# Kernel optimization log

Hardware: AMD Instinct MI355X
Metric: run time of the kernel (lower is better)

## Reference

```python
import jax, jax.numpy as jnp
import numpy as np

DN = ('NCHW', 'OIHW', 'NCHW')

def conv2d(x, w, b):
    y = jax.lax.conv_general_dilated(x, w, window_strides=(1, 1), padding='VALID', dimension_numbers=DN)
    return y + b[None, :, None, None]

def setup_inputs() -> dict:
    key = jax.random.key(0)
    ks = jax.random.split(key, 16)
    s = 0.02  # small init scale to keep relu chains numerically tame
    B, Cin, OUT = 128, 4, 9
    return {
        'state_m': jax.random.normal(ks[0], (B, Cin, 100, 100), jnp.float32),
        'state_g': jax.random.normal(ks[1], (B, 2), jnp.float32),
        'state_v': jax.random.normal(ks[2], (B, 2), jnp.float32),
        'conv1_w': jax.random.normal(ks[3], (32, Cin, 32, 32), jnp.float32) * s,
        'conv1_b': jnp.zeros((32,), jnp.float32),
        'conv2_w': jax.random.normal(ks[4], (64, 32, 32, 32), jnp.float32) * s,
        'conv2_b': jnp.zeros((64,), jnp.float32),
        'conv3_w': jax.random.normal(ks[5], (64, 64, 8, 8), jnp.float32) * s,
        'conv3_b': jnp.zeros((64,), jnp.float32),
        'conv4_w': jax.random.normal(ks[6], (64, 64, 8, 8), jnp.float32) * s,
        'conv4_b': jnp.zeros((64,), jnp.float32),
        'fc1_w': jax.random.normal(ks[7], (67, 4), jnp.float32) * s,
        'fc1_b': jnp.zeros((67,), jnp.float32),
        'fc2_w': jax.random.normal(ks[8], (512, 6400), jnp.float32) * s,
        'fc2_b': jnp.zeros((512,), jnp.float32),
        'fc3_w': jax.random.normal(ks[9], (512, 512), jnp.float32) * s,
        'fc3_b': jnp.zeros((512,), jnp.float32),
        'fc4_ea_w': jax.random.normal(ks[10], (OUT, 512), jnp.float32) * s,
        'fc4_ea_b': jnp.zeros((OUT,), jnp.float32),
        'fc4_ev_w': jax.random.normal(ks[11], (1, 512), jnp.float32) * s,
        'fc4_ev_b': jnp.zeros((1,), jnp.float32),
    }

def reference(state_m, state_g, state_v,
              conv1_w, conv1_b, conv2_w, conv2_b, conv3_w, conv3_b, conv4_w, conv4_b,
              fc1_w, fc1_b, fc2_w, fc2_b, fc3_w, fc3_b,
              fc4_ea_w, fc4_ea_b, fc4_ev_w, fc4_ev_b):
    x_m = jax.nn.relu(conv2d(state_m, conv1_w, conv1_b))   # [B,32,69,69]
    x_m = jax.nn.relu(conv2d(x_m, conv2_w, conv2_b))       # [B,64,38,38]
    x_m = jax.nn.relu(conv2d(x_m, conv3_w, conv3_b))       # [B,64,31,31]
    x_gv_ = jax.nn.relu(jnp.concatenate([state_g, state_v], axis=1) @ fc1_w.T + fc1_b)  # [B,67]
    convw = x_m.shape[2]  # 31
    # Torch loop overwrites x_gv each iteration: final tile is filled with x_gv_[0, convw-1]
    scalar = x_gv_[0, convw - 1]
    x_pls = x_m + scalar  # broadcast add (the CPU round-trip tile in torch)
    x_pls = jax.nn.relu(conv2d(x_pls, conv4_w, conv4_b))   # [B,64,24,24]
    x_pls = jax.nn.relu(conv2d(x_pls, conv4_w, conv4_b))   # [B,64,17,17]
    x_pls = jax.nn.relu(conv2d(x_pls, conv4_w, conv4_b))   # [B,64,10,10]
    x = x_pls.reshape(x_pls.shape[0], -1)                  # [B,6400]
    x = jax.nn.relu(x @ fc2_w.T + fc2_b)
    x = jax.nn.relu(x @ fc3_w.T + fc3_b)
    adv = x @ fc4_ea_w.T + fc4_ea_b                        # [B,outputs]
    val = x @ fc4_ev_w.T + fc4_ev_b                        # [B,1]
    return adv + val - jnp.mean(adv, axis=1, keepdims=True)
```

## Files before the change

### kernel.cpp

```cpp
#include <hip/hip_runtime.h>
#include <stdint.h>


using bf16_t = __bf16;
using bf16x8 = __attribute__((ext_vector_type(8))) __bf16;
using bf16x4 = __attribute__((ext_vector_type(4))) __bf16;
using f32x4  = __attribute__((ext_vector_type(4))) float;
using f32x16 = __attribute__((ext_vector_type(16))) float;

__device__ __forceinline__ f32x4 mfma16(bf16x8 a, bf16x8 b, f32x4 c) {
    return __builtin_amdgcn_mfma_f32_16x16x32_bf16(a, b, c, 0, 0, 0);
}
__device__ __forceinline__ f32x16 mfma32(bf16x8 a, bf16x8 b, f32x16 c) {
    return __builtin_amdgcn_mfma_f32_32x32x16_bf16(a, b, c, 0, 0, 0);
}

template<bool A16>
__device__ __forceinline__ bf16x8 load_frag(const bf16_t* p) {
    if constexpr (A16) {
        return *reinterpret_cast<const bf16x8*>(p);
    } else {
        union { bf16x8 v; uint64_t u[2]; } r;
        r.u[0] = *reinterpret_cast<const uint64_t*>(p);
        r.u[1] = *reinterpret_cast<const uint64_t*>(p + 4);
        return r.v;
    }
}

template<int CIN>
__global__ void pack_w(const float* __restrict__ src, bf16_t* __restrict__ dst,
                       int COUT, int KK) {
    int total = COUT * KK;
    for (int t = blockIdx.x * blockDim.x + threadIdx.x; t < total;
         t += gridDim.x * blockDim.x) {
        int cout = t / KK;
        int khw  = t - cout * KK;
        alignas(16) bf16_t tmp[CIN];
        #pragma unroll
        for (int c = 0; c < CIN; ++c)
            tmp[c] = (bf16_t)src[((size_t)cout * CIN + c) * KK + khw];
        bf16_t* d = dst + (size_t)t * CIN;
        if constexpr (CIN == 1) {
            d[0] = tmp[0];
        } else if constexpr (CIN == 4) {
            *reinterpret_cast<uint2*>(d) = *reinterpret_cast<const uint2*>(tmp);
        } else {
            #pragma unroll
            for (int c = 0; c < CIN; c += 8)
                *reinterpret_cast<uint4*>(d + c) =
                    *reinterpret_cast<const uint4*>(tmp + c);
        }
    }
}

template<int CIN, int COUT, int K>
__global__ void pack_wA(const float* __restrict__ src, bf16_t* __restrict__ dst) {
    constexpr int S  = K * CIN / 16;
    constexpr int NT = COUT / 32;
    int t = blockIdx.x * 256 + threadIdx.x;
    int l  = t & 63;
    int f  = t >> 6;
    int n  = f % NT;
    int fs = f / NT;
    int s  = fs % S;
    int kh = fs / S;
    if (kh >= K) return;
    int cout = n * 32 + (l & 31);
    int k0   = s * 16 + (l >> 5) * 8;
    alignas(16) bf16_t tmp[8];
    #pragma unroll
    for (int e = 0; e < 8; ++e) {
        int k   = k0 + e;
        int kw  = k / CIN;
        int cin = k % CIN;
        tmp[e] = (bf16_t)src[(((size_t)cout * CIN + cin) * K + kh) * K + kw];
    }
    *reinterpret_cast<uint4*>(dst + (size_t)t * 8) =
        *reinterpret_cast<const uint4*>(tmp);
}

__global__ void fc1_scalar(const float* __restrict__ g, const float* __restrict__ v,
                           const float* __restrict__ w, const float* __restrict__ b,
                           float* __restrict__ outp) {
    if (threadIdx.x == 0 && blockIdx.x == 0) {
        float s = b[30] + g[0] * w[120] + g[1] * w[121] + v[0] * w[122] + v[1] * w[123];
        *outp = s > 0.f ? s : 0.f;
    }
}

template<int CIN, int COUT, int W, int K, int OW, int WMT, int NSLOT,
         int ADD_SCALAR>
__global__ __launch_bounds__(256, 2) void conv_rr(
    const bf16_t* __restrict__ in, const bf16_t* __restrict__ wA,
    const float* __restrict__ bias, bf16_t* __restrict__ out,
    const float* __restrict__ scal) {
    constexpr int  P     = OW * OW;
    constexpr int  PIXB  = CIN * 2;
    constexpr int  ROWB  = W * PIXB;
    constexpr bool TR    = (CIN >= 16);
    constexpr int  NCH   = TR ? PIXB / 16 : 1;
    constexpr int  SPP   = TR ? NCH / 2 : 1;
    constexpr int  PS    = TR ? (W + 1) * 16 : 0;
    constexpr int  SLOTB = TR ? NCH * PS : ROWB;
    constexpr int  LDSB  = NSLOT * SLOTB;
    constexpr int  S     = K * CIN / 16;
    constexpr int  NT    = COUT / 32;
    constexpr int  BPX   = WMT * 32 * 4;
    constexpr int  CH    = ROWB / 16;
    constexpr int  NLD   = (CH + 255) / 256;
    __shared__ __align__(16) char smem[LDSB];

    const int tid  = threadIdx.x;
    const int wave = tid >> 6, lane = tid & 63;
    const int l31  = lane & 31, h = lane >> 5;
    const int img  = blockIdx.z;
    const int p0   = blockIdx.x * BPX;

    const char* inb = (const char*)(in + (size_t)img * ((size_t)W * W * CIN));

    const int r0 = p0 / OW;
    int plast = p0 + BPX - 1; if (plast > P - 1) plast = P - 1;
    const int r1 = plast / OW;

    int woff[NLD];
    #pragma unroll
    for (int i = 0; i < NLD; ++i) {
        int c = i * 256 + tid;
        if (c < CH) woff[i] = TR ? (c % NCH) * PS + (c / NCH) * 16 : c * 16;
        else        woff[i] = 0;
    }

    int pix[WMT], ldsadr[WMT];
    #pragma unroll
    for (int m = 0; m < WMT; ++m) {
        int p  = p0 + (wave * WMT + m) * 32 + l31;
        pix[m] = p;
        int pc = p < P ? p : P - 1;
        int oh = pc / OW;
        int ow = pc - oh * OW;
        ldsadr[m] = (oh % NSLOT) * SLOTB +
                    (TR ? ow * 16 + h * PS : ow * PIXB + h * 16);
    }

    for (int r = r0; r <= r1; ++r) {
        const char* g = inb + (size_t)r * ROWB;
        int base = (r % NSLOT) * SLOTB;
        for (int c = tid; c < CH; c += 256) {
            bf16x8 v = *reinterpret_cast<const bf16x8*>(g + c * 16);
            int off = TR ? (c % NCH) * PS + (c / NCH) * 16 : c * 16;
            *reinterpret_cast<bf16x8*>(smem + base + off) = v;
        }
    }
    __syncthreads();

    f32x16 acc[WMT][NT] = {};

    int wsl = (r1 + 1) % NSLOT;
    const char* gpre = inb + (size_t)(r1 + 1) * ROWB;
    const bf16_t* wl = wA + lane * 8;

    for (int kh = 0; kh < K; ++kh) {
        bf16x8 stv[NLD];
        const bool pf = kh < K - 1;
        if (pf) {
            #pragma unroll
            for (int i = 0; i < NLD; ++i) {
                int c = i * 256 + tid;
                if (c < CH) stv[i] = *reinterpret_cast<const bf16x8*>(gpre + c * 16);
            }
        }
        const bf16_t* ap = wl + (size_t)kh * (S * NT * 512);

        auto bread = [&](int m, int s) -> bf16x8 {
            int a = TR ? ldsadr[m] + (s % SPP) * (2 * PS) + (s / SPP) * 16
                       : ldsadr[m] + s * 32;
            return *reinterpret_cast<const bf16x8*>(smem + a);
        };
        bf16x8 bcur[WMT], acur[NT];
        #pragma unroll
        for (int m = 0; m < WMT; ++m) bcur[m] = bread(m, 0);
        #pragma unroll
        for (int n = 0; n < NT; ++n)
            acur[n] = *reinterpret_cast<const bf16x8*>(ap + n * 512);

        #pragma unroll 8
        for (int s = 0; s < S - 1; ++s) {
            bf16x8 bnx[WMT], anx[NT];
            #pragma unroll
            for (int m = 0; m < WMT; ++m) bnx[m] = bread(m, s + 1);
            #pragma unroll
            for (int n = 0; n < NT; ++n)
                anx[n] = *reinterpret_cast<const bf16x8*>(ap + ((s + 1) * NT + n) * 512);
            #pragma unroll
            for (int m = 0; m < WMT; ++m)
                #pragma unroll
                for (int n = 0; n < NT; ++n)
                    acc[m][n] = mfma32(acur[n], bcur[m], acc[m][n]);
            #pragma unroll
            for (int m = 0; m < WMT; ++m) bcur[m] = bnx[m];
            #pragma unroll
            for (int n = 0; n < NT; ++n) acur[n] = anx[n];
        }
        #pragma unroll
        for (int m = 0; m < WMT; ++m)
            #pragma unroll
            for (int n = 0; n < NT; ++n)
                acc[m][n] = mfma32(acur[n], bcur[m], acc[m][n]);

        if (pf) {
            int wb0 = wsl * SLOTB;
            #pragma unroll
            for (int i = 0; i < NLD; ++i) {
                int c = i * 256 + tid;
                if (c < CH)
                    *reinterpret_cast<bf16x8*>(smem + wb0 + woff[i]) = stv[i];
            }
            gpre += ROWB;
            wsl = (wsl + 1 == NSLOT) ? 0 : wsl + 1;
        }
        __syncthreads();
        #pragma unroll
        for (int m = 0; m < WMT; ++m) {
            int a2 = ldsadr[m] + SLOTB;
            ldsadr[m] = a2 >= LDSB ? a2 - LDSB : a2;
        }
    }

    float sc = 0.f;
    if constexpr (ADD_SCALAR) sc = *scal;
    bf16_t* outb = out + (size_t)img * ((size_t)P * COUT);
    #pragma unroll
    for (int m = 0; m < WMT; ++m) {
        if (pix[m] < P) {
            #pragma unroll
            for (int n = 0; n < NT; ++n) {
                #pragma unroll
                for (int rg = 0; rg < 4; ++rg) {
                    int cb = n * 32 + rg * 8 + h * 4;
                    f32x4 bv = *reinterpret_cast<const f32x4*>(bias + cb);
                    union { bf16x4 v; uint2 u; } o;
                    #pragma unroll
                    for (int j = 0; j < 4; ++j) {
                        float x = acc[m][n][rg * 4 + j] + bv[j];
                        x = x > 0.f ? x : 0.f;
                        x += sc;
                        o.v[j] = (bf16_t)x;
                    }
                    *reinterpret_cast<uint2*>(outb + (size_t)pix[m] * COUT + cb) = o.u;
                }
            }
        }
    }
}

template<int CIN, int COUT, int W, int K, int OW, int NBLK, int WMT,
         int ADD_SCALAR, bool A16>
__global__ __launch_bounds__(256, 2) void conv_mfma(
    const bf16_t* __restrict__ in, const bf16_t* __restrict__ wp,
    const float* __restrict__ bias, bf16_t* __restrict__ out,
    const float* __restrict__ scal) {
    constexpr int P    = OW * OW;
    constexpr int KCIN = K * CIN;
    constexpr int KTOT = K * KCIN;
    constexpr int RS   = KCIN / 32;
    constexpr int NT   = NBLK / 16;
    constexpr int BMT  = WMT * 4;

    const int b     = blockIdx.z;
    const int cout0 = blockIdx.y * NBLK;
    const int wave  = threadIdx.x >> 6;
    const int lane  = threadIdx.x & 63;
    const int l15   = lane & 15;
    const int l4    = lane >> 4;
    const int mt0   = blockIdx.x * BMT + wave * WMT;

    const bf16_t* inb = in + (size_t)b * (W * W * CIN);

    int      pix[WMT];
    uint32_t pb[WMT];
    #pragma unroll
    for (int m = 0; m < WMT; ++m) {
        int p  = (mt0 + m) * 16 + l15;
        pix[m] = p;
        int pc = p < P ? p : P - 1;
        int oh = pc / OW;
        int ow = pc - oh * OW;
        pb[m]  = (uint32_t)(oh * W + ow) * CIN;
    }
    uint32_t wb[NT];
    #pragma unroll
    for (int n = 0; n < NT; ++n)
        wb[n] = (uint32_t)(cout0 + n * 16 + l15) * KTOT + (uint32_t)l4 * 8u;

    f32x4 acc[WMT][NT];
    #pragma unroll
    for (int m = 0; m < WMT; ++m)
        #pragma unroll
        for (int n = 0; n < NT; ++n)
            acc[m][n] = f32x4{0.f, 0.f, 0.f, 0.f};

    uint32_t bofs = (uint32_t)l4 * 8u;
    for (int kh = 0; kh < K; ++kh) {
        #pragma unroll
        for (int s = 0; s < RS; ++s) {
            bf16x8 af[NT];
            #pragma unroll
            for (int n = 0; n < NT; ++n)
                af[n] = load_frag<true>(wp + wb[n] + kh * KCIN + s * 32);
            #pragma unroll
            for (int m = 0; m < WMT; ++m) {
                bf16x8 bfr = load_frag<A16>(inb + pb[m] + bofs + s * 32);
                #pragma unroll
                for (int n = 0; n < NT; ++n)
                    acc[m][n] = mfma16(af[n], bfr, acc[m][n]);
            }
        }
        bofs += (uint32_t)(W * CIN);
    }

    float sc = 0.f;
    if constexpr (ADD_SCALAR) sc = *scal;
    bf16_t* outb = out + (size_t)b * P * COUT;
    #pragma unroll
    for (int n = 0; n < NT; ++n) {
        const int cb = cout0 + n * 16 + l4 * 4;
        f32x4 bv = *reinterpret_cast<const f32x4*>(bias + cb);
        #pragma unroll
        for (int m = 0; m < WMT; ++m) {
            if (pix[m] < P) {
                f32x4 v = acc[m][n];
                union { bf16x4 h; uint2 u; } st;
                #pragma unroll
                for (int r = 0; r < 4; ++r) {
                    float x = v[r] + bv[r];
                    x = x > 0.f ? x : 0.f;
                    x += sc;
                    st.h[r] = (bf16_t)x;
                }
                *reinterpret_cast<uint2*>(outb + (size_t)pix[m] * COUT + cb) = st.u;
            }
        }
    }
}

__global__ __launch_bounds__(256, 2) void fc2_kernel(
    const bf16_t* __restrict__ x, const bf16_t* __restrict__ w,
    float* __restrict__ part) {
    const int nb = blockIdx.x, kc = blockIdx.y;
    const int wave = threadIdx.x >> 6, lane = threadIdx.x & 63;
    const int l15 = lane & 15, l4 = lane >> 4;
    const int wm = wave & 1, wn = wave >> 1;

    f32x4 acc[4][2];
    #pragma unroll
    for (int m = 0; m < 4; ++m)
        #pragma unroll
        for (int n = 0; n < 2; ++n) acc[m][n] = f32x4{0.f, 0.f, 0.f, 0.f};

    uint32_t xb[4], wbf[2];
    #pragma unroll
    for (int m = 0; m < 4; ++m)
        xb[m] = (uint32_t)(16 * (wm * 4 + m) + l15) * 6400u + kc * 1600u + l4 * 8u;
    #pragma unroll
    for (int n = 0; n < 2; ++n)
        wbf[n] = (uint32_t)(nb * 64 + wn * 32 + n * 16 + l15) * 6400u + kc * 1600u + l4 * 8u;

    for (int s = 0; s < 50; ++s) {
        bf16x8 af[2];
        #pragma unroll
        for (int n = 0; n < 2; ++n)
            af[n] = load_frag<true>(w + wbf[n] + s * 32);
        #pragma unroll
        for (int m = 0; m < 4; ++m) {
            bf16x8 bfr = load_frag<true>(x + xb[m] + s * 32);
            #pragma unroll
            for (int n = 0; n < 2; ++n)
                acc[m][n] = mfma16(af[n], bfr, acc[m][n]);
        }
    }
    #pragma unroll
    for (int m = 0; m < 4; ++m) {
        int bcol = 16 * (wm * 4 + m) + l15;
        #pragma unroll
        for (int n = 0; n < 2; ++n) {
            int cf = nb * 64 + wn * 32 + n * 16 + l4 * 4;
            *reinterpret_cast<f32x4*>(part + ((size_t)kc * 128 + bcol) * 512 + cf) =
                acc[m][n];
        }
    }
}

__global__ void fc2_reduce(const float* __restrict__ part,
                           const float* __restrict__ bias,
                           bf16_t* __restrict__ xo) {
    int t = blockIdx.x * 256 + threadIdx.x;
    if (t < 128 * 512) {
        int b = t >> 9, co = t & 511;
        float s = bias[co];
        #pragma unroll
        for (int kc = 0; kc < 4; ++kc) s += part[((size_t)kc * 128 + b) * 512 + co];
        xo[t] = (bf16_t)(s > 0.f ? s : 0.f);
    }
}

__global__ __launch_bounds__(256, 2) void fc3_kernel(
    const bf16_t* __restrict__ x, const bf16_t* __restrict__ w,
    const float* __restrict__ bias, bf16_t* __restrict__ xo) {
    const int nb = blockIdx.x;
    const int wave = threadIdx.x >> 6, lane = threadIdx.x & 63;
    const int l15 = lane & 15, l4 = lane >> 4;

    f32x4 acc[2][4];
    #pragma unroll
    for (int m = 0; m < 2; ++m)
        #pragma unroll
        for (int n = 0; n < 4; ++n) acc[m][n] = f32x4{0.f, 0.f, 0.f, 0.f};

    uint32_t xb[2], wbf[4];
    #pragma unroll
    for (int m = 0; m < 2; ++m)
        xb[m] = (uint32_t)(16 * (wave * 2 + m) + l15) * 512u + l4 * 8u;
    #pragma unroll
    for (int n = 0; n < 4; ++n)
        wbf[n] = (uint32_t)(nb * 64 + n * 16 + l15) * 512u + l4 * 8u;

    #pragma unroll
    for (int s = 0; s < 16; ++s) {
        bf16x8 af[4];
        #pragma unroll
        for (int n = 0; n < 4; ++n) af[n] = load_frag<true>(w + wbf[n] + s * 32);
        #pragma unroll
        for (int m = 0; m < 2; ++m) {
            bf16x8 bfr = load_frag<true>(x + xb[m] + s * 32);
            #pragma unroll
            for (int n = 0; n < 4; ++n)
                acc[m][n] = mfma16(af[n], bfr, acc[m][n]);
        }
    }
    #pragma unroll
    for (int n = 0; n < 4; ++n) {
        int cf = nb * 64 + n * 16 + l4 * 4;
        f32x4 bv = *reinterpret_cast<const f32x4*>(bias + cf);
        #pragma unroll
        for (int m = 0; m < 2; ++m) {
            int brow = 16 * (wave * 2 + m) + l15;
            union { bf16x4 h; uint2 u; } st;
            #pragma unroll
            for (int r = 0; r < 4; ++r) {
                float v = acc[m][n][r] + bv[r];
                st.h[r] = (bf16_t)(v > 0.f ? v : 0.f);
            }
            *reinterpret_cast<uint2*>(xo + (size_t)brow * 512 + cf) = st.u;
        }
    }
}

__global__ void final_kernel(const bf16_t* __restrict__ x,
                             const float* __restrict__ eaw, const float* __restrict__ eab,
                             const float* __restrict__ evw, const float* __restrict__ evb,
                             float* __restrict__ out) {
    int b = blockIdx.x, lane = threadIdx.x;
    bf16x8 xv = *reinterpret_cast<const bf16x8*>(x + (size_t)b * 512 + lane * 8);
    float xs[8];
    #pragma unroll
    for (int i = 0; i < 8; ++i) xs[i] = (float)xv[i];
    float a[10];
    #pragma unroll
    for (int j = 0; j < 10; ++j) {
        const float* wr = (j < 9) ? (eaw + (size_t)j * 512) : evw;
        const f32x4* w4 = reinterpret_cast<const f32x4*>(wr + lane * 8);
        f32x4 w0 = w4[0], w1 = w4[1];
        float s = 0.f;
        #pragma unroll
        for (int i = 0; i < 4; ++i) s += xs[i] * w0[i];
        #pragma unroll
        for (int i = 0; i < 4; ++i) s += xs[4 + i] * w1[i];
        a[j] = s;
    }
    #pragma unroll
    for (int off = 1; off < 64; off <<= 1)
        #pragma unroll
        for (int j = 0; j < 10; ++j) a[j] += __shfl_xor(a[j], off);
    if (lane < 9) {
        float val  = a[9] + evb[0];
        float mean = 0.f;
        #pragma unroll
        for (int j = 0; j < 9; ++j) mean += a[j] + eab[j];
        mean *= (1.f / 9.f);
        out[b * 9 + lane] = a[lane] + eab[lane] + val - mean;
    }
}

extern "C" void kernel_launch(void* const* d_in, const int* in_sizes, int n_in,
                              void* d_out, int out_size, void* d_ws, size_t ws_size,
                              hipStream_t stream) {
    const float* state_m  = (const float*)d_in[0];
    const float* state_g  = (const float*)d_in[1];
    const float* state_v  = (const float*)d_in[2];
    const float* conv1_w  = (const float*)d_in[3];
    const float* conv1_b  = (const float*)d_in[4];
    const float* conv2_w  = (const float*)d_in[5];
    const float* conv2_b  = (const float*)d_in[6];
    const float* conv3_w  = (const float*)d_in[7];
    const float* conv3_b  = (const float*)d_in[8];
    const float* conv4_w  = (const float*)d_in[9];
    const float* conv4_b  = (const float*)d_in[10];
    const float* fc1_w    = (const float*)d_in[11];
    const float* fc1_b    = (const float*)d_in[12];
    const float* fc2_w    = (const float*)d_in[13];
    const float* fc2_b    = (const float*)d_in[14];
    const float* fc3_w    = (const float*)d_in[15];
    const float* fc3_b    = (const float*)d_in[16];
    const float* fc4_ea_w = (const float*)d_in[17];
    const float* fc4_ea_b = (const float*)d_in[18];
    const float* fc4_ev_w = (const float*)d_in[19];
    const float* fc4_ev_b = (const float*)d_in[20];

    char* ws = (char*)d_ws;
    bf16_t* w1A    = (bf16_t*)(ws + 0);
    bf16_t* w2A    = (bf16_t*)(ws + 262144);
    bf16_t* w3A    = (bf16_t*)(ws + 4456448);
    bf16_t* w4A    = (bf16_t*)(ws + 4980736);
    bf16_t* w4p    = (bf16_t*)(ws + 5505024);
    bf16_t* fc2wp  = (bf16_t*)(ws + 6029312);
    bf16_t* fc3wp  = (bf16_t*)(ws + 12582912);
    float*  scal   = (float*) (ws + 13107200);
    float*  part   = (float*) (ws + 13107456);
    bf16_t* x2fc   = (bf16_t*)(ws + 14156032);
    bf16_t* x3fc   = (bf16_t*)(ws + 14287104);
    bf16_t* a0     = (bf16_t*)(ws + 14418176);
    bf16_t* x4a    = (bf16_t*)(ws + 14418176);
    bf16_t* x1     = (bf16_t*)(ws + 24658176);
    bf16_t* x4b    = (bf16_t*)(ws + 24658176);
    bf16_t* x4c    = (bf16_t*)(ws + 29393152);
    bf16_t* x2     = (bf16_t*)(ws + 63660288);
    bf16_t* x3     = (bf16_t*)(ws + 87318784);
    (void)in_sizes; (void)n_in; (void)out_size; (void)ws_size;

    pack_wA<4, 32, 32> <<<dim3(64),   256, 0, stream>>>(conv1_w, w1A);
    pack_wA<32, 64, 32><<<dim3(1024), 256, 0, stream>>>(conv2_w, w2A);
    pack_wA<64, 64, 8> <<<dim3(128),  256, 0, stream>>>(conv3_w, w3A);
    pack_wA<64, 64, 8> <<<dim3(128),  256, 0, stream>>>(conv4_w, w4A);
    pack_w<64><<<dim3(16),   256, 0, stream>>>(conv4_w, w4p, 64, 64);
    pack_w<64><<<dim3(200),  256, 0, stream>>>(fc2_w, fc2wp, 512, 100);
    pack_w<1> <<<dim3(1024), 256, 0, stream>>>(fc3_w, fc3wp, 512, 512);
    pack_w<4> <<<dim3(1024), 256, 0, stream>>>(state_m, a0, 128, 10000);
    fc1_scalar<<<1, 64, 0, stream>>>(state_g, state_v, fc1_w, fc1_b, scal);

    conv_rr<4, 32, 100, 32, 69, 3, 8, 0>
        <<<dim3(13, 1, 128), 256, 0, stream>>>(a0, w1A, conv1_b, x1, nullptr);
    conv_rr<32, 64, 69, 32, 38, 3, 12, 0>
        <<<dim3(4, 1, 128), 256, 0, stream>>>(x1, w2A, conv2_b, x2, nullptr);
    conv_rr<64, 64, 38, 8, 31, 2, 11, 1>
        <<<dim3(4, 1, 128), 256, 0, stream>>>(x2, w3A, conv3_b, x3, scal);
    conv_rr<64, 64, 31, 8, 24, 2, 13, 0>
        <<<dim3(3, 1, 128), 256, 0, stream>>>(x3, w4A, conv4_b, x4a, nullptr);
    conv_rr<64, 64, 24, 8, 17, 2, 17, 0>
        <<<dim3(2, 1, 128), 256, 0, stream>>>(x4a, w4A, conv4_b, x4b, nullptr);
    conv_mfma<64, 64, 17, 8, 10, 32, 1, 0, true>
        <<<dim3(2, 2, 128), 256, 0, stream>>>(x4b, w4p, conv4_b, x4c, nullptr);

    fc2_kernel<<<dim3(8, 4), 256, 0, stream>>>(x4c, fc2wp, part);
    fc2_reduce<<<dim3(256), 256, 0, stream>>>(part, fc2_b, x2fc);
    fc3_kernel<<<dim3(8), 256, 0, stream>>>(x2fc, fc3wp, fc3_b, x3fc);
    final_kernel<<<dim3(128), 64, 0, stream>>>(x3fc, fc4_ea_w, fc4_ea_b,
                                               fc4_ev_w, fc4_ev_b, (float*)d_out);
}
```

Measured before the change: 1.293 ms.

## Deepen conv inner-loop prefetch to four stages, pad LDS slots, raise MFMA priority

Replaces the double-buffered fragment loads in the conv kernel's reduction loop with a four-deep rotating register pipeline, so LDS and weight loads are issued three steps ahead of their MFMAs. MFMA blocks are wrapped in s_setprio to favour matrix issue over other waves. LDS row slots are padded to a 128-byte-aligned offset relative to the pixel stride to reduce bank conflicts. This costs more VGPRs, which under launch_bounds(256,2) could cause spills. The unrolled schedule also assumes S is a multiple of 4 and at least 4.

```diff
diff --git a/kernel.cpp b/kernel.cpp
--- a/kernel.cpp
+++ b/kernel.cpp
@@ -101,7 +101,9 @@
     constexpr int  NCH   = TR ? PIXB / 16 : 1;
     constexpr int  SPP   = TR ? NCH / 2 : 1;
     constexpr int  PS    = TR ? (W + 1) * 16 : 0;
-    constexpr int  SLOTB = TR ? NCH * PS : ROWB;
+    constexpr int  SLOTB0 = TR ? NCH * PS : ROWB;
+    constexpr int  PADB  = TR ? ((16 * OW - SLOTB0) % 128 + 128) % 128 : 0;
+    constexpr int  SLOTB = SLOTB0 + PADB;
     constexpr int  LDSB  = NSLOT * SLOTB;
     constexpr int  S     = K * CIN / 16;
     constexpr int  NT    = COUT / 32;
@@ -171,41 +173,48 @@
         }
         const bf16_t* ap = wl + (size_t)kh * (S * NT * 512);
 
-        auto bread = [&](int m, int s) -> bf16x8 {
-            int a = TR ? ldsadr[m] + (s % SPP) * (2 * PS) + (s / SPP) * 16
-                       : ldsadr[m] + s * 32;
-            return *reinterpret_cast<const bf16x8*>(smem + a);
-        };
-        bf16x8 bcur[WMT], acur[NT];
-        #pragma unroll
-        for (int m = 0; m < WMT; ++m) bcur[m] = bread(m, 0);
-        #pragma unroll
-        for (int n = 0; n < NT; ++n)
-            acur[n] = *reinterpret_cast<const bf16x8*>(ap + n * 512);
-
-        #pragma unroll 8
-        for (int s = 0; s < S - 1; ++s) {
-            bf16x8 bnx[WMT], anx[NT];
-            #pragma unroll
-            for (int m = 0; m < WMT; ++m) bnx[m] = bread(m, s + 1);
-            #pragma unroll
-            for (int n = 0; n < NT; ++n)
-                anx[n] = *reinterpret_cast<const bf16x8*>(ap + ((s + 1) * NT + n) * 512);
-            #pragma unroll
-            for (int m = 0; m < WMT; ++m)
-                #pragma unroll
-                for (int n = 0; n < NT; ++n)
-                    acc[m][n] = mfma32(acur[n], bcur[m], acc[m][n]);
-            #pragma unroll
-            for (int m = 0; m < WMT; ++m) bcur[m] = bnx[m];
-            #pragma unroll
-            for (int n = 0; n < NT; ++n) acur[n] = anx[n];
-        }
-        #pragma unroll
-        for (int m = 0; m < WMT; ++m)
-            #pragma unroll
-            for (int n = 0; n < NT; ++n)
-                acc[m][n] = mfma32(acur[n], bcur[m], acc[m][n]);
+        bf16x8 bS0[WMT], bS1[WMT], bS2[WMT], bS3[WMT];
+        bf16x8 aS0[NT],  aS1[NT],  aS2[NT],  aS3[NT];
+
+#define LOADSET(BS, AS, SIDX)                                               \
+        {                                                                   \
+            const int _s = (SIDX);                                          \
+            _Pragma("unroll")                                               \
+            for (int m = 0; m < WMT; ++m) {                                 \
+                int a = TR ? ldsadr[m] + (_s % SPP) * (2 * PS) + (_s / SPP) * 16 \
+                           : ldsadr[m] + _s * 32;                           \
+                BS[m] = *reinterpret_cast<const bf16x8*>(smem + a);         \
+            }                                                               \
+            _Pragma("unroll")                                               \
+            for (int n = 0; n < NT; ++n)                                    \
+                AS[n] = *reinterpret_cast<const bf16x8*>(ap + (_s * NT + n) * 512); \
+        }
+#define MFMASET(BS, AS)                                                     \
+        {                                                                   \
+            __builtin_amdgcn_s_setprio(1);                                  \
+            _Pragma("unroll")                                               \
+            for (int m = 0; m < WMT; ++m)                                   \
+                _Pragma("unroll")                                           \
+                for (int n = 0; n < NT; ++n)                                \
+                    acc[m][n] = mfma32(AS[n], BS[m], acc[m][n]);            \
+            __builtin_amdgcn_s_setprio(0);                                  \
+        }
+
+        LOADSET(bS0, aS0, 0)
+        LOADSET(bS1, aS1, 1)
+        LOADSET(bS2, aS2, 2)
+        for (int sb = 0; sb + 8 <= S; sb += 4) {
+            MFMASET(bS0, aS0)  LOADSET(bS3, aS3, sb + 3)
+            MFMASET(bS1, aS1)  LOADSET(bS0, aS0, sb + 4)
+            MFMASET(bS2, aS2)  LOADSET(bS1, aS1, sb + 5)
+            MFMASET(bS3, aS3)  LOADSET(bS2, aS2, sb + 6)
+        }
+        MFMASET(bS0, aS0)  LOADSET(bS3, aS3, S - 1)
+        MFMASET(bS1, aS1)
+        MFMASET(bS2, aS2)
+        MFMASET(bS3, aS3)
+#undef LOADSET
+#undef MFMASET
 
         if (pf) {
             int wb0 = wsl * SLOTB;
```

Result: slower. 1.518 ms (+17.4%).

## Deepen conv2 operand prefetch to four stages, pad LDS slots, retile conv2

Applied to the files above, without the earlier changes.

Adds a DEPTH template parameter. With DEPTH=4 the inner K loop keeps four rotating register sets of LDS B-fragments and global A-fragments, loading three steps ahead of the MFMAs, and raises wave priority around each MFMA group. LDS slot size is padded to shift bank alignment of the transposed layout. Conv2 moves to WMT=2, 9 slots and 6 blocks per image, which gives more blocks but less reuse per block. The deeper pipeline raises register pressure, which may lower occupancy under the 256x2 launch bounds.

```diff
diff --git a/kernel.cpp b/kernel.cpp
--- a/kernel.cpp
+++ b/kernel.cpp
@@ -89,7 +89,7 @@
 }
 
 template<int CIN, int COUT, int W, int K, int OW, int WMT, int NSLOT,
-         int ADD_SCALAR>
+         int ADD_SCALAR, int DEPTH>
 __global__ __launch_bounds__(256, 2) void conv_rr(
     const bf16_t* __restrict__ in, const bf16_t* __restrict__ wA,
     const float* __restrict__ bias, bf16_t* __restrict__ out,
@@ -101,7 +101,9 @@
     constexpr int  NCH   = TR ? PIXB / 16 : 1;
     constexpr int  SPP   = TR ? NCH / 2 : 1;
     constexpr int  PS    = TR ? (W + 1) * 16 : 0;
-    constexpr int  SLOTB = TR ? NCH * PS : ROWB;
+    constexpr int  SLOTB0 = TR ? NCH * PS : ROWB;
+    constexpr int  PADB  = TR ? ((16 * OW - SLOTB0) % 128 + 128) % 128 : 0;
+    constexpr int  SLOTB = SLOTB0 + PADB;
     constexpr int  LDSB  = NSLOT * SLOTB;
     constexpr int  S     = K * CIN / 16;
     constexpr int  NT    = COUT / 32;
@@ -171,41 +173,86 @@
         }
         const bf16_t* ap = wl + (size_t)kh * (S * NT * 512);
 
-        auto bread = [&](int m, int s) -> bf16x8 {
-            int a = TR ? ldsadr[m] + (s % SPP) * (2 * PS) + (s / SPP) * 16
-                       : ldsadr[m] + s * 32;
-            return *reinterpret_cast<const bf16x8*>(smem + a);
-        };
-        bf16x8 bcur[WMT], acur[NT];
-        #pragma unroll
-        for (int m = 0; m < WMT; ++m) bcur[m] = bread(m, 0);
-        #pragma unroll
-        for (int n = 0; n < NT; ++n)
-            acur[n] = *reinterpret_cast<const bf16x8*>(ap + n * 512);
-
-        #pragma unroll 8
-        for (int s = 0; s < S - 1; ++s) {
-            bf16x8 bnx[WMT], anx[NT];
-            #pragma unroll
-            for (int m = 0; m < WMT; ++m) bnx[m] = bread(m, s + 1);
+        if constexpr (DEPTH == 4) {
+            bf16x8 bS0[WMT], bS1[WMT], bS2[WMT], bS3[WMT];
+            bf16x8 aS0[NT],  aS1[NT],  aS2[NT],  aS3[NT];
+
+#define LOADSET(BS, AS, SIDX)                                               \
+            {                                                               \
+                const int _s = (SIDX);                                      \
+                _Pragma("unroll")                                           \
+                for (int m = 0; m < WMT; ++m) {                             \
+                    int a = TR ? ldsadr[m] + (_s % SPP) * (2 * PS) + (_s / SPP) * 16 \
+                               : ldsadr[m] + _s * 32;                       \
+                    BS[m] = *reinterpret_cast<const bf16x8*>(smem + a);     \
+                }                                                           \
+                _Pragma("unroll")                                           \
+                for (int n = 0; n < NT; ++n)                                \
+                    AS[n] = *reinterpret_cast<const bf16x8*>(ap + (_s * NT + n) * 512); \
+            }
+#define MFMASET(BS, AS)                                                     \
+            {                                                               \
+                __builtin_amdgcn_s_setprio(1);                              \
+                _Pragma("unroll")                                           \
+                for (int m = 0; m < WMT; ++m)                               \
+                    _Pragma("unroll")                                       \
+                    for (int n = 0; n < NT; ++n)                            \
+                        acc[m][n] = mfma32(AS[n], BS[m], acc[m][n]);        \
+                __builtin_amdgcn_s_setprio(0);                              \
+            }
+
+            LOADSET(bS0, aS0, 0)
+            LOADSET(bS1, aS1, 1)
+            LOADSET(bS2, aS2, 2)
+            for (int sb = 0; sb + 8 <= S; sb += 4) {
+                MFMASET(bS0, aS0)  LOADSET(bS3, aS3, sb + 3)
+                MFMASET(bS1, aS1)  LOADSET(bS0, aS0, sb + 4)
+                MFMASET(bS2, aS2)  LOADSET(bS1, aS1, sb + 5)
+                MFMASET(bS3, aS3)  LOADSET(bS2, aS2, sb + 6)
+            }
+            MFMASET(bS0, aS0)  LOADSET(bS3, aS3, S - 1)
+            MFMASET(bS1, aS1)
+            MFMASET(bS2, aS2)
+            MFMASET(bS3, aS3)
+#undef LOADSET
+#undef MFMASET
+        } else {
+            auto bread = [&](int m, int s) -> bf16x8 {
+                int a = TR ? ldsadr[m] + (s % SPP) * (2 * PS) + (s / SPP) * 16
+                           : ldsadr[m] + s * 32;
+                return *reinterpret_cast<const bf16x8*>(smem + a);
+            };
+            bf16x8 bcur[WMT], acur[NT];
+            #pragma unroll
+            for (int m = 0; m < WMT; ++m) bcur[m] = bread(m, 0);
             #pragma unroll
             for (int n = 0; n < NT; ++n)
-                anx[n] = *reinterpret_cast<const bf16x8*>(ap + ((s + 1) * NT + n) * 512);
+                acur[n] = *reinterpret_cast<const bf16x8*>(ap + n * 512);
+
+            #pragma unroll 8
+            for (int s = 0; s < S - 1; ++s) {
+                bf16x8 bnx[WMT], anx[NT];
+                #pragma unroll
+                for (int m = 0; m < WMT; ++m) bnx[m] = bread(m, s + 1);
+                #pragma unroll
+                for (int n = 0; n < NT; ++n)
+                    anx[n] = *reinterpret_cast<const bf16x8*>(ap + ((s + 1) * NT + n) * 512);
+                #pragma unroll
+                for (int m = 0; m < WMT; ++m)
+                    #pragma unroll
+                    for (int n = 0; n < NT; ++n)
+                        acc[m][n] = mfma32(acur[n], bcur[m], acc[m][n]);
+                #pragma unroll
+                for (int m = 0; m < WMT; ++m) bcur[m] = bnx[m];
+                #pragma unroll
+                for (int n = 0; n < NT; ++n) acur[n] = anx[n];
+            }
             #pragma unroll
             for (int m = 0; m < WMT; ++m)
                 #pragma unroll
                 for (int n = 0; n < NT; ++n)
                     acc[m][n] = mfma32(acur[n], bcur[m], acc[m][n]);
-            #pragma unroll
-            for (int m = 0; m < WMT; ++m) bcur[m] = bnx[m];
-            #pragma unroll
-            for (int n = 0; n < NT; ++n) acur[n] = anx[n];
-        }
-        #pragma unroll
-        for (int m = 0; m < WMT; ++m)
-            #pragma unroll
-            for (int n = 0; n < NT; ++n)
-                acc[m][n] = mfma32(acur[n], bcur[m], acc[m][n]);
+        }
 
         if (pf) {
             int wb0 = wsl * SLOTB;
@@ -547,15 +594,15 @@
     pack_w<4> <<<dim3(1024), 256, 0, stream>>>(state_m, a0, 128, 10000);
     fc1_scalar<<<1, 64, 0, stream>>>(state_g, state_v, fc1_w, fc1_b, scal);
 
-    conv_rr<4, 32, 100, 32, 69, 3, 8, 0>
+    conv_rr<4, 32, 100, 32, 69, 3, 8, 0, 1>
         <<<dim3(13, 1, 128), 256, 0, stream>>>(a0, w1A, conv1_b, x1, nullptr);
-    conv_rr<32, 64, 69, 32, 38, 3, 12, 0>
-        <<<dim3(4, 1, 128), 256, 0, stream>>>(x1, w2A, conv2_b, x2, nullptr);
-    conv_rr<64, 64, 38, 8, 31, 2, 11, 1>
+    conv_rr<32, 64, 69, 32, 38, 2, 9, 0, 4>
+        <<<dim3(6, 1, 128), 256, 0, stream>>>(x1, w2A, conv2_b, x2, nullptr);
+    conv_rr<64, 64, 38, 8, 31, 2, 11, 1, 1>
         <<<dim3(4, 1, 128), 256, 0, stream>>>(x2, w3A, conv3_b, x3, scal);
-    conv_rr<64, 64, 31, 8, 24, 2, 13, 0>
+    conv_rr<64, 64, 31, 8, 24, 2, 13, 0, 1>
         <<<dim3(3, 1, 128), 256, 0, stream>>>(x3, w4A, conv4_b, x4a, nullptr);
-    conv_rr<64, 64, 24, 8, 17, 2, 17, 0>
+    conv_rr<64, 64, 24, 8, 17, 2, 17, 0, 1>
         <<<dim3(2, 1, 128), 256, 0, stream>>>(x4a, w4A, conv4_b, x4b, nullptr);
     conv_mfma<64, 64, 17, 8, 10, 32, 1, 0, true>
         <<<dim3(2, 2, 128), 256, 0, stream>>>(x4b, w4p, conv4_b, x4c, nullptr);
```

Measured after the change: 1.213 ms. 6.2% less time.
